# Optimization experiments

Measured on AMD Instinct MI355X. Metric: run time of the kernel, lower is better.

The kernel has to match this reference:

```python
import jax, jax.numpy as jnp
import numpy as np
from jax import lax

M0 = 131072      # total atoms
N_ONEHOT = 92    # one-hot width
N_ENV = 55       # env feature width (so 3*(92-19)+55 = 274 -> final flat dim 324)
N_CRYSTALS = 4096


def _conv1d(x, w, b):
    # x: [N, Cin, L], w: [Cout, Cin, K] -> [N, Cout, L-K+1] (VALID, stride 1)
    y = lax.conv_general_dilated(x, w, window_strides=(1,), padding='VALID',
                                 dimension_numbers=('NCH', 'OIH', 'NCH'))
    return y + b[None, :, None]


def _maxpool2(x):
    # MaxPool1d(kernel=2, stride=2) over last dim
    return lax.reduce_window(x, -jnp.inf, lax.max, (1, 1, 2), (1, 1, 2), 'VALID')


def setup_inputs() -> dict:
    key = jax.random.key(0)
    ks = jax.random.split(key, 12)
    inp = {
        'atom_one_hot': jax.random.uniform(ks[0], (M0, N_ONEHOT), jnp.float32),
        'atom_env': jax.random.normal(ks[1], (M0, N_ENV), jnp.float32),
        'crystal_atom_idx': jnp.sort(jax.random.randint(ks[2], (M0,), 0, N_CRYSTALS)),
        'num_segments': N_CRYSTALS,
        # parameters (PyTorch-style fan-in scaled init)
        'conva_w': jax.random.normal(ks[3], (3, 1, 20), jnp.float32) * 0.2,
        'conva_b': jax.random.normal(ks[4], (3,), jnp.float32) * 0.1,
        'conv1_w': jax.random.normal(ks[5], (3, 1, 20), jnp.float32) * 0.2,
        'conv1_b': jax.random.normal(ks[6], (3,), jnp.float32) * 0.1,
        'conv2_w': jax.random.normal(ks[7], (6, 3, 20), jnp.float32) * 0.1,
        'conv2_b': jax.random.normal(ks[8], (6,), jnp.float32) * 0.1,
        'lin_w': jax.random.normal(ks[9], (32, 324), jnp.float32) * 0.05,
        'lin_b': jnp.zeros((32,), jnp.float32),
        'lin1_w': jax.random.normal(ks[10], (1, 32), jnp.float32) * 0.15,
        'lin1_b': jnp.zeros((1,), jnp.float32),
    }
    return inp


def reference(atom_one_hot, atom_env, crystal_atom_idx, num_segments,
              conva_w, conva_b, conv1_w, conv1_b, conv2_w, conv2_b,
              lin_w, lin_b, lin1_w, lin1_b):
    m0 = atom_one_hot.shape[0]
    # per-atom conv over the one-hot vector
    atom = jax.nn.relu(_conv1d(atom_one_hot[:, None, :], conva_w, conva_b))
    atom = atom.reshape(m0, -1)                       # [m0, 3*(n0-19)]
    total = jnp.concatenate([atom, atom_env], axis=1)[:, None, :]  # [m0, 1, 274]
    one = _maxpool2(jax.nn.relu(_conv1d(total, conv1_w, conv1_b)))   # [m0, 3, 127]
    one = _maxpool2(jax.nn.relu(_conv1d(one, conv2_w, conv2_b)))     # [m0, 6, 54]
    one = one.reshape(m0, -1)                          # [m0, 324]
    # ragged per-crystal mean (segment mean) == sum_atom
    sums = jax.ops.segment_sum(one, crystal_atom_idx, num_segments=num_segments)
    counts = jax.ops.segment_sum(jnp.ones((m0,), one.dtype), crystal_atom_idx,
                                 num_segments=num_segments)
    pooled = sums / jnp.maximum(counts, 1.0)[:, None]  # [n_crystals, 324]
    pooled = jax.nn.relu(pooled)
    h = jax.nn.softplus(pooled @ lin_w.T + lin_b)      # [n_crystals, 32]
    return h @ lin1_w.T + lin1_b                       # [n_crystals, 1]
```

## Files before the change

### kernel.cpp

```cpp
#include <hip/hip_runtime.h>
#include <math.h>

#define M0 131072
#define NC 4096
#define FDIM 324
#define APW 4

#define DSWIN21(w0, w1, w2, w3, w4, g, addr)                                   \
  asm volatile("ds_read2_b64 %0, %6 offset0:0 offset1:1\n\t"                   \
               "ds_read2_b64 %1, %6 offset0:2 offset1:3\n\t"                   \
               "ds_read2_b64 %2, %6 offset0:4 offset1:5\n\t"                   \
               "ds_read2_b64 %3, %6 offset0:6 offset1:7\n\t"                   \
               "ds_read2_b64 %4, %6 offset0:8 offset1:9\n\t"                   \
               "ds_read_b32 %5, %6 offset:80\n\t"                              \
               "s_waitcnt lgkmcnt(0)"                                          \
               : "=v"(w0), "=v"(w1), "=v"(w2), "=v"(w3), "=v"(w4), "=v"(g)     \
               : "v"(addr))

#define DSWIN24(w0, w1, w2, w3, w4, w5, addr)                                  \
  asm volatile("ds_read_b128 %0, %6 offset:0\n\t"                              \
               "ds_read_b128 %1, %6 offset:16\n\t"                             \
               "ds_read_b128 %2, %6 offset:32\n\t"                             \
               "ds_read_b128 %3, %6 offset:48\n\t"                             \
               "ds_read_b128 %4, %6 offset:64\n\t"                             \
               "ds_read_b128 %5, %6 offset:80\n\t"                             \
               "s_waitcnt lgkmcnt(0)"                                          \
               : "=v"(w0), "=v"(w1), "=v"(w2), "=v"(w3), "=v"(w4), "=v"(w5)    \
               : "v"(addr))

#define DSWQ5(q0, q1, q2, q3, q4, addr)                                        \
  asm volatile("ds_read_b128 %0, %5 offset:0\n\t"                              \
               "ds_read_b128 %1, %5 offset:16\n\t"                             \
               "ds_read_b128 %2, %5 offset:32\n\t"                             \
               "ds_read_b128 %3, %5 offset:48\n\t"                             \
               "ds_read_b128 %4, %5 offset:64\n\t"                             \
               "s_waitcnt lgkmcnt(0)"                                          \
               : "=v"(q0), "=v"(q1), "=v"(q2), "=v"(q3), "=v"(q4)              \
               : "v"(addr))

#define DSW64(addr, val)  asm volatile("ds_write_b64 %0, %1" :: "v"(addr), "v"(val))
#define DSW32(addr, val)  asm volatile("ds_write_b32 %0, %1" :: "v"(addr), "v"(val))

template<int J>
__device__ __forceinline__ float el21(const float4 (&W)[5], float g) {
    if constexpr (J >= 20) return g;
    else {
        constexpr int q = J >> 2, r = J & 3;
        if constexpr (r == 0) return W[q].x;
        else if constexpr (r == 1) return W[q].y;
        else if constexpr (r == 2) return W[q].z;
        else return W[q].w;
    }
}
template<int J>
__device__ __forceinline__ float el24(const float4 (&W)[6]) {
    constexpr int q = J >> 2, r = J & 3;
    if constexpr (r == 0) return W[q].x;
    else if constexpr (r == 1) return W[q].y;
    else if constexpr (r == 2) return W[q].z;
    else return W[q].w;
}

template<int K0>
__device__ __forceinline__ void fq2(const float4 wq, const float4 (&W)[5], float g,
                                    float& a0, float& a1) {
    a0 = fmaf(el21<K0 + 0>(W, g), wq.x, a0); a1 = fmaf(el21<K0 + 1>(W, g), wq.x, a1);
    a0 = fmaf(el21<K0 + 1>(W, g), wq.y, a0); a1 = fmaf(el21<K0 + 2>(W, g), wq.y, a1);
    a0 = fmaf(el21<K0 + 2>(W, g), wq.z, a0); a1 = fmaf(el21<K0 + 3>(W, g), wq.z, a1);
    a0 = fmaf(el21<K0 + 3>(W, g), wq.w, a0); a1 = fmaf(el21<K0 + 4>(W, g), wq.w, a1);
}
template<int K0>
__device__ __forceinline__ void fq4(const float4 wq, const float4 (&W)[6], float (&a)[4]) {
    a[0] = fmaf(el24<K0 + 0>(W), wq.x, a[0]); a[1] = fmaf(el24<K0 + 1>(W), wq.x, a[1]);
    a[2] = fmaf(el24<K0 + 2>(W), wq.x, a[2]); a[3] = fmaf(el24<K0 + 3>(W), wq.x, a[3]);
    a[0] = fmaf(el24<K0 + 1>(W), wq.y, a[0]); a[1] = fmaf(el24<K0 + 2>(W), wq.y, a[1]);
    a[2] = fmaf(el24<K0 + 3>(W), wq.y, a[2]); a[3] = fmaf(el24<K0 + 4>(W), wq.y, a[3]);
    a[0] = fmaf(el24<K0 + 2>(W), wq.z, a[0]); a[1] = fmaf(el24<K0 + 3>(W), wq.z, a[1]);
    a[2] = fmaf(el24<K0 + 4>(W), wq.z, a[2]); a[3] = fmaf(el24<K0 + 5>(W), wq.z, a[3]);
    a[0] = fmaf(el24<K0 + 3>(W), wq.w, a[0]); a[1] = fmaf(el24<K0 + 4>(W), wq.w, a[1]);
    a[2] = fmaf(el24<K0 + 5>(W), wq.w, a[2]); a[3] = fmaf(el24<K0 + 6>(W), wq.w, a[3]);
}

__global__ __launch_bounds__(256, 8) void atom_kernel(
    const float* __restrict__ oh_g,
    const float* __restrict__ env_g,
    const int*   __restrict__ idx_g,
    const float* __restrict__ wA, const float* __restrict__ bA,
    const float* __restrict__ w1, const float* __restrict__ b1,
    const float* __restrict__ w2, const float* __restrict__ b2,
    float* __restrict__ sums,
    float* __restrict__ counts)
{
    __shared__ __align__(16) float w_lds[480];
    __shared__ __align__(16) float s_total[4][280];
    __shared__ __align__(16) float s_one1[4][384];

    const int wave = threadIdx.x >> 6;
    const int lane = threadIdx.x & 63;
    const int tid  = threadIdx.x;

    const unsigned w_b   = (unsigned)(size_t)w_lds;
    const unsigned wD_b  = w_b + 480u;
    const unsigned tot_b = (unsigned)(size_t)s_total[wave];
    const unsigned one_b = (unsigned)(size_t)s_one1[wave];
    const unsigned oh_b  = one_b;

    for (int i = tid; i < 360; i += 256) DSW32(w_b + (120u + (unsigned)i) * 4u, w2[i]);
    if (tid < 60)       DSW32(w_b + (unsigned)tid * 4u, wA[tid]);
    else if (tid < 120) DSW32(w_b + (unsigned)tid * 4u, w1[tid - 60]);
    __syncthreads();

    const int wbase = (blockIdx.x * 4 + wave) * APW;

    float fa[6] = {0.f, 0.f, 0.f, 0.f, 0.f, 0.f};
    float cnt = 0.f;
    int cur = idx_g[wbase];

    for (int it = 0; it < APW; ++it) {
        const int atom = wbase + it;
        const int cry = idx_g[atom];
        if (cry != cur) {
            if (lane < 54) {
                float* dst = sums + (size_t)cur * FDIM + lane;
                #pragma unroll
                for (int c2 = 0; c2 < 6; ++c2) {
                    atomicAdd(dst + c2 * 54, fa[c2]);
                    fa[c2] = 0.f;
                }
            }
            if (lane == 0) atomicAdd(&counts[cur], cnt);
            cnt = 0.f;
            cur = cry;
        }

        if (lane < 46) {
            const float2 v = *reinterpret_cast<const float2*>(oh_g + (size_t)atom * 92 + 2 * lane);
            DSW64(oh_b + (unsigned)lane * 8u, v);
        }
        if (lane < 55) {
            const float e = env_g[(size_t)atom * 55 + lane];
            DSW32(tot_b + (219u + (unsigned)lane) * 4u, e);
        }

        if (lane < 37) {
            float4 W[5]; float g;
            DSWIN21(W[0], W[1], W[2], W[3], W[4], g, oh_b + (unsigned)lane * 8u);
            const unsigned p2 = 2u * (unsigned)lane;
            #pragma unroll
            for (int c = 0; c < 3; ++c) {
                float4 wq[5];
                DSWQ5(wq[0], wq[1], wq[2], wq[3], wq[4], w_b + (unsigned)c * 80u);
                float a0 = bA[c], a1 = a0;
                fq2<0>(wq[0], W, g, a0, a1);  fq2<4>(wq[1], W, g, a0, a1);
                fq2<8>(wq[2], W, g, a0, a1);  fq2<12>(wq[3], W, g, a0, a1);
                fq2<16>(wq[4], W, g, a0, a1);
                const unsigned tb = tot_b + (73u * (unsigned)c + p2) * 4u;
                DSW32(tb, fmaxf(a0, 0.f));
                if (p2 + 1 < 73) DSW32(tb + 4u, fmaxf(a1, 0.f));
            }
        }

        {
            float4 W[6];
            DSWIN24(W[0], W[1], W[2], W[3], W[4], W[5], tot_b + (unsigned)lane * 16u);
            #pragma unroll
            for (int c = 0; c < 3; ++c) {
                float4 wq[5];
                DSWQ5(wq[0], wq[1], wq[2], wq[3], wq[4], w_b + 240u + (unsigned)c * 80u);
                float a4[4] = {b1[c], b1[c], b1[c], b1[c]};
                fq4<0>(wq[0], W, a4);  fq4<4>(wq[1], W, a4);  fq4<8>(wq[2], W, a4);
                fq4<12>(wq[3], W, a4); fq4<16>(wq[4], W, a4);
                float2 st;
                st.x = fmaxf(fmaxf(a4[0], a4[1]), 0.f);
                st.y = fmaxf(fmaxf(a4[2], a4[3]), 0.f);
                DSW64(one_b + ((unsigned)c * 128u + 2u * (unsigned)lane) * 4u, st);
            }
        }

        if (lane < 54) {
            float acc0[6], acc1[6];
            #pragma unroll
            for (int c2 = 0; c2 < 6; ++c2) { acc0[c2] = b2[c2]; acc1[c2] = acc0[c2]; }
            #pragma unroll
            for (int ch = 0; ch < 3; ++ch) {
                float4 W[5]; float g;
                DSWIN21(W[0], W[1], W[2], W[3], W[4], g,
                        one_b + (unsigned)ch * 512u + (unsigned)lane * 8u);
                #pragma unroll
                for (int c2 = 0; c2 < 6; ++c2) {
                    float4 wq[5];
                    DSWQ5(wq[0], wq[1], wq[2], wq[3], wq[4],
                          wD_b + ((unsigned)c2 * 3u + (unsigned)ch) * 80u);
                    fq2<0>(wq[0], W, g, acc0[c2], acc1[c2]);
                    fq2<4>(wq[1], W, g, acc0[c2], acc1[c2]);
                    fq2<8>(wq[2], W, g, acc0[c2], acc1[c2]);
                    fq2<12>(wq[3], W, g, acc0[c2], acc1[c2]);
                    fq2<16>(wq[4], W, g, acc0[c2], acc1[c2]);
                }
            }
            #pragma unroll
            for (int c2 = 0; c2 < 6; ++c2)
                fa[c2] += fmaxf(fmaxf(acc0[c2], acc1[c2]), 0.f);
        }
        cnt += 1.f;
    }

    if (lane < 54) {
        float* dst = sums + (size_t)cur * FDIM + lane;
        #pragma unroll
        for (int c2 = 0; c2 < 6; ++c2) atomicAdd(dst + c2 * 54, fa[c2]);
    }
    if (lane == 0) atomicAdd(&counts[cur], cnt);
}

__global__ __launch_bounds__(64) void head_kernel(
    const float* __restrict__ sums, const float* __restrict__ counts,
    const float* __restrict__ lin_w, const float* __restrict__ lin_b,
    const float* __restrict__ lin1_w, const float* __restrict__ lin1_b,
    float* __restrict__ out)
{
    __shared__ float p[FDIM];
    const int c = blockIdx.x;
    const int lane = threadIdx.x;
    const float inv = 1.0f / fmaxf(counts[c], 1.0f);
    for (int i = lane; i < FDIM; i += 64)
        p[i] = fmaxf(sums[(size_t)c * FDIM + i] * inv, 0.f);
    __syncthreads();

    float r = 0.f;
    if (lane < 32) {
        float acc = lin_b[lane];
        const float* wrow = lin_w + lane * FDIM;
        #pragma unroll 4
        for (int i = 0; i < FDIM; ++i) acc = fmaf(p[i], wrow[i], acc);
        const float sp = (acc > 0.f) ? acc + log1pf(expf(-acc)) : log1pf(expf(acc));
        r = sp * lin1_w[lane];
    }
    #pragma unroll
    for (int off = 16; off; off >>= 1) r += __shfl_down(r, off);
    if (lane == 0) out[c] = r + lin1_b[0];
}

extern "C" void kernel_launch(void* const* d_in, const int* in_sizes, int n_in,
                              void* d_out, int out_size, void* d_ws, size_t ws_size,
                              hipStream_t stream) {
    (void)in_sizes; (void)n_in; (void)out_size; (void)ws_size;
    const float* oh    = (const float*)d_in[0];
    const float* env   = (const float*)d_in[1];
    const int*   idx   = (const int*)  d_in[2];
    const float* wA    = (const float*)d_in[4];
    const float* bA    = (const float*)d_in[5];
    const float* w1    = (const float*)d_in[6];
    const float* b1    = (const float*)d_in[7];
    const float* w2    = (const float*)d_in[8];
    const float* b2    = (const float*)d_in[9];
    const float* lin_w = (const float*)d_in[10];
    const float* lin_b = (const float*)d_in[11];
    const float* lin1_w= (const float*)d_in[12];
    const float* lin1_b= (const float*)d_in[13];

    float* sums   = (float*)d_ws;
    float* counts = sums + (size_t)NC * FDIM;

    hipMemsetAsync(d_ws, 0, ((size_t)NC * FDIM + NC) * sizeof(float), stream);

    atom_kernel<<<M0 / (4 * APW), 256, 0, stream>>>(oh, env, idx, wA, bA, w1, b1,
                                                    w2, b2, sums, counts);
    head_kernel<<<NC, 64, 0, stream>>>(sums, counts, lin_w, lin_b, lin1_w, lin1_b,
                                       (float*)d_out);
}
```

Before: 249.3 us.

## Load conv weights via scalar loads into SGPRs instead of LDS broadcast reads

Conv weights are no longer staged in LDS with a block-wide barrier. Each 20-tap filter is now fetched with s_load_dwordx16/x4 into scalar registers and used directly as the uniform FMA operand, which removes the per-lane ds_read_b128 weight traffic and the __syncthreads. The block index is also remapped (blockIdx&7)*1024+(blockIdx>>3), which changes which atoms neighbouring blocks process and may affect cache and atomic locality across XCDs. Each scalar load waits on lgkmcnt(0), so its latency is exposed, and the larger SGPR demand could hurt scheduling.

```diff
diff --git a/kernel.cpp b/kernel.cpp
--- a/kernel.cpp
+++ b/kernel.cpp
@@ -5,6 +5,9 @@
 #define NC 4096
 #define FDIM 324
 #define APW 4
+
+typedef __attribute__((ext_vector_type(16))) float f32x16;
+typedef __attribute__((ext_vector_type(4)))  float f32x4s;
 
 #define DSWIN21(w0, w1, w2, w3, w4, g, addr)                                   \
   asm volatile("ds_read2_b64 %0, %6 offset0:0 offset1:1\n\t"                   \
@@ -28,18 +31,15 @@
                : "=v"(w0), "=v"(w1), "=v"(w2), "=v"(w3), "=v"(w4), "=v"(w5)    \
                : "v"(addr))
 
-#define DSWQ5(q0, q1, q2, q3, q4, addr)                                        \
-  asm volatile("ds_read_b128 %0, %5 offset:0\n\t"                              \
-               "ds_read_b128 %1, %5 offset:16\n\t"                             \
-               "ds_read_b128 %2, %5 offset:32\n\t"                             \
-               "ds_read_b128 %3, %5 offset:48\n\t"                             \
-               "ds_read_b128 %4, %5 offset:64\n\t"                             \
-               "s_waitcnt lgkmcnt(0)"                                          \
-               : "=v"(q0), "=v"(q1), "=v"(q2), "=v"(q3), "=v"(q4)              \
-               : "v"(addr))
-
 #define DSW64(addr, val)  asm volatile("ds_write_b64 %0, %1" :: "v"(addr), "v"(val))
 #define DSW32(addr, val)  asm volatile("ds_write_b32 %0, %1" :: "v"(addr), "v"(val))
+
+#define SLDW20(d16, d4, ptr, O16, O4)                                          \
+  asm volatile("s_load_dwordx16 %0, %2, %3\n\t"                                \
+               "s_load_dwordx4 %1, %2, %4\n\t"                                 \
+               "s_waitcnt lgkmcnt(0)"                                          \
+               : "=&s"(d16), "=&s"(d4)                                         \
+               : "s"(ptr), "n"(O16), "n"(O4))
 
 template<int J>
 __device__ __forceinline__ float el21(const float4 (&W)[5], float g) {
@@ -61,24 +61,48 @@
     else return W[q].w;
 }
 
-template<int K0>
-__device__ __forceinline__ void fq2(const float4 wq, const float4 (&W)[5], float g,
-                                    float& a0, float& a1) {
-    a0 = fmaf(el21<K0 + 0>(W, g), wq.x, a0); a1 = fmaf(el21<K0 + 1>(W, g), wq.x, a1);
-    a0 = fmaf(el21<K0 + 1>(W, g), wq.y, a0); a1 = fmaf(el21<K0 + 2>(W, g), wq.y, a1);
-    a0 = fmaf(el21<K0 + 2>(W, g), wq.z, a0); a1 = fmaf(el21<K0 + 3>(W, g), wq.z, a1);
-    a0 = fmaf(el21<K0 + 3>(W, g), wq.w, a0); a1 = fmaf(el21<K0 + 4>(W, g), wq.w, a1);
-}
-template<int K0>
-__device__ __forceinline__ void fq4(const float4 wq, const float4 (&W)[6], float (&a)[4]) {
-    a[0] = fmaf(el24<K0 + 0>(W), wq.x, a[0]); a[1] = fmaf(el24<K0 + 1>(W), wq.x, a[1]);
-    a[2] = fmaf(el24<K0 + 2>(W), wq.x, a[2]); a[3] = fmaf(el24<K0 + 3>(W), wq.x, a[3]);
-    a[0] = fmaf(el24<K0 + 1>(W), wq.y, a[0]); a[1] = fmaf(el24<K0 + 2>(W), wq.y, a[1]);
-    a[2] = fmaf(el24<K0 + 3>(W), wq.y, a[2]); a[3] = fmaf(el24<K0 + 4>(W), wq.y, a[3]);
-    a[0] = fmaf(el24<K0 + 2>(W), wq.z, a[0]); a[1] = fmaf(el24<K0 + 3>(W), wq.z, a[1]);
-    a[2] = fmaf(el24<K0 + 4>(W), wq.z, a[2]); a[3] = fmaf(el24<K0 + 5>(W), wq.z, a[3]);
-    a[0] = fmaf(el24<K0 + 3>(W), wq.w, a[0]); a[1] = fmaf(el24<K0 + 4>(W), wq.w, a[1]);
-    a[2] = fmaf(el24<K0 + 5>(W), wq.w, a[2]); a[3] = fmaf(el24<K0 + 6>(W), wq.w, a[3]);
+template<int K>
+__device__ __forceinline__ void sfq2(const float wk, const float4 (&W)[5], float g,
+                                     float& a0, float& a1) {
+    a0 = fmaf(el21<K>(W, g),     wk, a0);
+    a1 = fmaf(el21<K + 1>(W, g), wk, a1);
+}
+template<int K>
+__device__ __forceinline__ void sfq4(const float wk, const float4 (&W)[6], float (&a)[4]) {
+    a[0] = fmaf(el24<K>(W),     wk, a[0]);
+    a[1] = fmaf(el24<K + 1>(W), wk, a[1]);
+    a[2] = fmaf(el24<K + 2>(W), wk, a[2]);
+    a[3] = fmaf(el24<K + 3>(W), wk, a[3]);
+}
+
+#define SFQ20_2(S16, S4, W, g, a0, a1) do {                                    \
+  sfq2<0>(S16[0],W,g,a0,a1);  sfq2<1>(S16[1],W,g,a0,a1);                       \
+  sfq2<2>(S16[2],W,g,a0,a1);  sfq2<3>(S16[3],W,g,a0,a1);                       \
+  sfq2<4>(S16[4],W,g,a0,a1);  sfq2<5>(S16[5],W,g,a0,a1);                       \
+  sfq2<6>(S16[6],W,g,a0,a1);  sfq2<7>(S16[7],W,g,a0,a1);                       \
+  sfq2<8>(S16[8],W,g,a0,a1);  sfq2<9>(S16[9],W,g,a0,a1);                       \
+  sfq2<10>(S16[10],W,g,a0,a1); sfq2<11>(S16[11],W,g,a0,a1);                    \
+  sfq2<12>(S16[12],W,g,a0,a1); sfq2<13>(S16[13],W,g,a0,a1);                    \
+  sfq2<14>(S16[14],W,g,a0,a1); sfq2<15>(S16[15],W,g,a0,a1);                    \
+  sfq2<16>(S4[0],W,g,a0,a1);  sfq2<17>(S4[1],W,g,a0,a1);                       \
+  sfq2<18>(S4[2],W,g,a0,a1);  sfq2<19>(S4[3],W,g,a0,a1); } while (0)
+
+#define SFQ20_4(S16, S4, W, a) do {                                            \
+  sfq4<0>(S16[0],W,a);  sfq4<1>(S16[1],W,a);  sfq4<2>(S16[2],W,a);             \
+  sfq4<3>(S16[3],W,a);  sfq4<4>(S16[4],W,a);  sfq4<5>(S16[5],W,a);             \
+  sfq4<6>(S16[6],W,a);  sfq4<7>(S16[7],W,a);  sfq4<8>(S16[8],W,a);             \
+  sfq4<9>(S16[9],W,a);  sfq4<10>(S16[10],W,a); sfq4<11>(S16[11],W,a);          \
+  sfq4<12>(S16[12],W,a); sfq4<13>(S16[13],W,a); sfq4<14>(S16[14],W,a);         \
+  sfq4<15>(S16[15],W,a); sfq4<16>(S4[0],W,a);  sfq4<17>(S4[1],W,a);            \
+  sfq4<18>(S4[2],W,a);  sfq4<19>(S4[3],W,a); } while (0)
+
+template<int IDX>
+__device__ __forceinline__ void d_one(const float* __restrict__ w2p,
+                                      const float4 (&W)[5], float g,
+                                      float& a0, float& a1) {
+    f32x16 s16; f32x4s s4;
+    SLDW20(s16, s4, w2p, IDX * 80, IDX * 80 + 64);
+    SFQ20_2(s16, s4, W, g, a0, a1);
 }
 
 __global__ __launch_bounds__(256, 8) void atom_kernel(
@@ -91,26 +115,20 @@
     float* __restrict__ sums,
     float* __restrict__ counts)
 {
-    __shared__ __align__(16) float w_lds[480];
     __shared__ __align__(16) float s_total[4][280];
     __shared__ __align__(16) float s_one1[4][384];
 
+    const int bid = (blockIdx.x & 7) * 1024 + (blockIdx.x >> 3);
+
     const int wave = threadIdx.x >> 6;
     const int lane = threadIdx.x & 63;
-    const int tid  = threadIdx.x;
-
-    const unsigned w_b   = (unsigned)(size_t)w_lds;
-    const unsigned wD_b  = w_b + 480u;
-    const unsigned tot_b = (unsigned)(size_t)s_total[wave];
-    const unsigned one_b = (unsigned)(size_t)s_one1[wave];
-    const unsigned oh_b  = one_b;
-
-    for (int i = tid; i < 360; i += 256) DSW32(w_b + (120u + (unsigned)i) * 4u, w2[i]);
-    if (tid < 60)       DSW32(w_b + (unsigned)tid * 4u, wA[tid]);
-    else if (tid < 120) DSW32(w_b + (unsigned)tid * 4u, w1[tid - 60]);
-    __syncthreads();
-
-    const int wbase = (blockIdx.x * 4 + wave) * APW;
+
+    const unsigned tot_b = (unsigned)(size_t)&s_total[wave][0];
+    const unsigned one_b = (unsigned)(size_t)&s_one1[wave][0];
+    const unsigned lane8  = (unsigned)lane * 8u;
+    const unsigned lane16 = (unsigned)lane * 16u;
+
+    const int wbase = (bid * 4 + wave) * APW;
 
     float fa[6] = {0.f, 0.f, 0.f, 0.f, 0.f, 0.f};
     float cnt = 0.f;
@@ -135,45 +153,74 @@
 
         if (lane < 46) {
             const float2 v = *reinterpret_cast<const float2*>(oh_g + (size_t)atom * 92 + 2 * lane);
-            DSW64(oh_b + (unsigned)lane * 8u, v);
+            DSW64(one_b + lane8, v);
         }
         if (lane < 55) {
-            const float e = env_g[(size_t)atom * 55 + lane];
-            DSW32(tot_b + (219u + (unsigned)lane) * 4u, e);
+            DSW32(tot_b + (219u + (unsigned)lane) * 4u, env_g[(size_t)atom * 55 + lane]);
         }
 
         if (lane < 37) {
             float4 W[5]; float g;
-            DSWIN21(W[0], W[1], W[2], W[3], W[4], g, oh_b + (unsigned)lane * 8u);
+            DSWIN21(W[0], W[1], W[2], W[3], W[4], g, one_b + lane8);
             const unsigned p2 = 2u * (unsigned)lane;
-            #pragma unroll
-            for (int c = 0; c < 3; ++c) {
-                float4 wq[5];
-                DSWQ5(wq[0], wq[1], wq[2], wq[3], wq[4], w_b + (unsigned)c * 80u);
-                float a0 = bA[c], a1 = a0;
-                fq2<0>(wq[0], W, g, a0, a1);  fq2<4>(wq[1], W, g, a0, a1);
-                fq2<8>(wq[2], W, g, a0, a1);  fq2<12>(wq[3], W, g, a0, a1);
-                fq2<16>(wq[4], W, g, a0, a1);
-                const unsigned tb = tot_b + (73u * (unsigned)c + p2) * 4u;
-                DSW32(tb, fmaxf(a0, 0.f));
-                if (p2 + 1 < 73) DSW32(tb + 4u, fmaxf(a1, 0.f));
+            {
+                f32x16 s16; f32x4s s4;
+                SLDW20(s16, s4, wA, 0, 64);
+                float a0 = bA[0], a1 = a0;
+                SFQ20_2(s16, s4, W, g, a0, a1);
+                DSW32(tot_b + p2 * 4u, fmaxf(a0, 0.f));
+                if (p2 + 1 < 73) DSW32(tot_b + (p2 + 1) * 4u, fmaxf(a1, 0.f));
+            }
+            {
+                f32x16 s16; f32x4s s4;
+                SLDW20(s16, s4, wA, 80, 144);
+                float a0 = bA[1], a1 = a0;
+                SFQ20_2(s16, s4, W, g, a0, a1);
+                DSW32(tot_b + (73u + p2) * 4u, fmaxf(a0, 0.f));
+                if (p2 + 1 < 73) DSW32(tot_b + (74u + p2) * 4u, fmaxf(a1, 0.f));
+            }
+            {
+                f32x16 s16; f32x4s s4;
+                SLDW20(s16, s4, wA, 160, 224);
+                float a0 = bA[2], a1 = a0;
+                SFQ20_2(s16, s4, W, g, a0, a1);
+                DSW32(tot_b + (146u + p2) * 4u, fmaxf(a0, 0.f));
+                if (p2 + 1 < 73) DSW32(tot_b + (147u + p2) * 4u, fmaxf(a1, 0.f));
             }
         }
 
         {
             float4 W[6];
-            DSWIN24(W[0], W[1], W[2], W[3], W[4], W[5], tot_b + (unsigned)lane * 16u);
-            #pragma unroll
-            for (int c = 0; c < 3; ++c) {
-                float4 wq[5];
-                DSWQ5(wq[0], wq[1], wq[2], wq[3], wq[4], w_b + 240u + (unsigned)c * 80u);
-                float a4[4] = {b1[c], b1[c], b1[c], b1[c]};
-                fq4<0>(wq[0], W, a4);  fq4<4>(wq[1], W, a4);  fq4<8>(wq[2], W, a4);
-                fq4<12>(wq[3], W, a4); fq4<16>(wq[4], W, a4);
+            DSWIN24(W[0], W[1], W[2], W[3], W[4], W[5], tot_b + lane16);
+            {
+                f32x16 s16; f32x4s s4;
+                SLDW20(s16, s4, w1, 0, 64);
+                float a4[4] = {b1[0], b1[0], b1[0], b1[0]};
+                SFQ20_4(s16, s4, W, a4);
                 float2 st;
                 st.x = fmaxf(fmaxf(a4[0], a4[1]), 0.f);
                 st.y = fmaxf(fmaxf(a4[2], a4[3]), 0.f);
-                DSW64(one_b + ((unsigned)c * 128u + 2u * (unsigned)lane) * 4u, st);
+                DSW64(one_b + (2u * (unsigned)lane) * 4u, st);
+            }
+            {
+                f32x16 s16; f32x4s s4;
+                SLDW20(s16, s4, w1, 80, 144);
+                float a4[4] = {b1[1], b1[1], b1[1], b1[1]};
+                SFQ20_4(s16, s4, W, a4);
+                float2 st;
+                st.x = fmaxf(fmaxf(a4[0], a4[1]), 0.f);
+                st.y = fmaxf(fmaxf(a4[2], a4[3]), 0.f);
+                DSW64(one_b + (128u + 2u * (unsigned)lane) * 4u, st);
+            }
+            {
+                f32x16 s16; f32x4s s4;
+                SLDW20(s16, s4, w1, 160, 224);
+                float a4[4] = {b1[2], b1[2], b1[2], b1[2]};
+                SFQ20_4(s16, s4, W, a4);
+                float2 st;
+                st.x = fmaxf(fmaxf(a4[0], a4[1]), 0.f);
+                st.y = fmaxf(fmaxf(a4[2], a4[3]), 0.f);
+                DSW64(one_b + (256u + 2u * (unsigned)lane) * 4u, st);
             }
         }
 
@@ -181,22 +228,35 @@
             float acc0[6], acc1[6];
             #pragma unroll
             for (int c2 = 0; c2 < 6; ++c2) { acc0[c2] = b2[c2]; acc1[c2] = acc0[c2]; }
-            #pragma unroll
-            for (int ch = 0; ch < 3; ++ch) {
+            {
                 float4 W[5]; float g;
-                DSWIN21(W[0], W[1], W[2], W[3], W[4], g,
-                        one_b + (unsigned)ch * 512u + (unsigned)lane * 8u);
-                #pragma unroll
-                for (int c2 = 0; c2 < 6; ++c2) {
-                    float4 wq[5];
-                    DSWQ5(wq[0], wq[1], wq[2], wq[3], wq[4],
-                          wD_b + ((unsigned)c2 * 3u + (unsigned)ch) * 80u);
-                    fq2<0>(wq[0], W, g, acc0[c2], acc1[c2]);
-                    fq2<4>(wq[1], W, g, acc0[c2], acc1[c2]);
-                    fq2<8>(wq[2], W, g, acc0[c2], acc1[c2]);
-                    fq2<12>(wq[3], W, g, acc0[c2], acc1[c2]);
-                    fq2<16>(wq[4], W, g, acc0[c2], acc1[c2]);
-                }
+                DSWIN21(W[0], W[1], W[2], W[3], W[4], g, one_b + lane8);
+                d_one<0>(w2, W, g, acc0[0], acc1[0]);
+                d_one<3>(w2, W, g, acc0[1], acc1[1]);
+                d_one<6>(w2, W, g, acc0[2], acc1[2]);
+                d_one<9>(w2, W, g, acc0[3], acc1[3]);
+                d_one<12>(w2, W, g, acc0[4], acc1[4]);
+                d_one<15>(w2, W, g, acc0[5], acc1[5]);
+            }
+            {
+                float4 W[5]; float g;
+                DSWIN21(W[0], W[1], W[2], W[3], W[4], g, one_b + 512u + lane8);
+                d_one<1>(w2, W, g, acc0[0], acc1[0]);
+                d_one<4>(w2, W, g, acc0[1], acc1[1]);
+                d_one<7>(w2, W, g, acc0[2], acc1[2]);
+                d_one<10>(w2, W, g, acc0[3], acc1[3]);
+                d_one<13>(w2, W, g, acc0[4], acc1[4]);
+                d_one<16>(w2, W, g, acc0[5], acc1[5]);
+            }
+            {
+                float4 W[5]; float g;
+                DSWIN21(W[0], W[1], W[2], W[3], W[4], g, one_b + 1024u + lane8);
+                d_one<2>(w2, W, g, acc0[0], acc1[0]);
+                d_one<5>(w2, W, g, acc0[1], acc1[1]);
+                d_one<8>(w2, W, g, acc0[2], acc1[2]);
+                d_one<11>(w2, W, g, acc0[3], acc1[3]);
+                d_one<14>(w2, W, g, acc0[4], acc1[4]);
+                d_one<17>(w2, W, g, acc0[5], acc1[5]);
             }
             #pragma unroll
             for (int c2 = 0; c2 < 6; ++c2)
@@ -264,8 +324,8 @@
 
     hipMemsetAsync(d_ws, 0, ((size_t)NC * FDIM + NC) * sizeof(float), stream);
 
-    atom_kernel<<<M0 / (4 * APW), 256, 0, stream>>>(oh, env, idx, wA, bA, w1, b1,
-                                                    w2, b2, sums, counts);
+    atom_kernel<<<M0 / 16, 256, 0, stream>>>(oh, env, idx, wA, bA, w1, b1,
+                                             w2, b2, sums, counts);
     head_kernel<<<NC, 64, 0, stream>>>(sums, counts, lin_w, lin_b, lin1_w, lin1_b,
                                        (float*)d_out);
 }
```

Measured after the change: 291.2 us. +16.8%, slower.

## Compute conv2 stage with bf16 MFMA instead of scalar FMAs

Applied to the files above, without the earlier changes.

Replaces the scalar FP32 conv2 (3->6 channels, kernel 20) with bf16 16x16x32 MFMA tiles. Conv1 outputs are packed to bf16 in LDS, and conv2 weights are preloaded as A-fragments in registers. Maxpool is done with a lane shuffle and results are staged through an LDS pool buffer before accumulation. Launch bounds occupancy drops from 8 to 4, and bf16 rounding of the activations and weights lowers accuracy.

```diff
diff --git a/kernel.cpp b/kernel.cpp
--- a/kernel.cpp
+++ b/kernel.cpp
@@ -5,6 +5,10 @@
 #define NC 4096
 #define FDIM 324
 #define APW 4
+
+typedef __attribute__((ext_vector_type(8))) short bf16x8;
+typedef __attribute__((ext_vector_type(4))) float f32x4;
+typedef __attribute__((ext_vector_type(4))) int   i32x4;
 
 #define DSWIN21(w0, w1, w2, w3, w4, g, addr)                                   \
   asm volatile("ds_read2_b64 %0, %6 offset0:0 offset1:1\n\t"                   \
@@ -14,7 +18,8 @@
                "ds_read2_b64 %4, %6 offset0:8 offset1:9\n\t"                   \
                "ds_read_b32 %5, %6 offset:80\n\t"                              \
                "s_waitcnt lgkmcnt(0)"                                          \
-               : "=v"(w0), "=v"(w1), "=v"(w2), "=v"(w3), "=v"(w4), "=v"(g)     \
+               : "=&v"(w0), "=&v"(w1), "=&v"(w2), "=&v"(w3), "=&v"(w4),        \
+                 "=&v"(g)                                                      \
                : "v"(addr))
 
 #define DSWIN24(w0, w1, w2, w3, w4, w5, addr)                                  \
@@ -25,21 +30,73 @@
                "ds_read_b128 %4, %6 offset:64\n\t"                             \
                "ds_read_b128 %5, %6 offset:80\n\t"                             \
                "s_waitcnt lgkmcnt(0)"                                          \
-               : "=v"(w0), "=v"(w1), "=v"(w2), "=v"(w3), "=v"(w4), "=v"(w5)    \
-               : "v"(addr))
-
-#define DSWQ5(q0, q1, q2, q3, q4, addr)                                        \
+               : "=&v"(w0), "=&v"(w1), "=&v"(w2), "=&v"(w3), "=&v"(w4),        \
+                 "=&v"(w5)                                                     \
+               : "v"(addr))
+
+#define DSWQ5(q, addr)                                                         \
   asm volatile("ds_read_b128 %0, %5 offset:0\n\t"                              \
                "ds_read_b128 %1, %5 offset:16\n\t"                             \
                "ds_read_b128 %2, %5 offset:32\n\t"                             \
                "ds_read_b128 %3, %5 offset:48\n\t"                             \
                "ds_read_b128 %4, %5 offset:64\n\t"                             \
                "s_waitcnt lgkmcnt(0)"                                          \
-               : "=v"(q0), "=v"(q1), "=v"(q2), "=v"(q3), "=v"(q4)              \
+               : "=&v"(q[0]), "=&v"(q[1]), "=&v"(q[2]), "=&v"(q[3]),           \
+                 "=&v"(q[4])                                                   \
+               : "v"(addr))
+
+#define DSB_G4(q00,q01,q02,q10,q11,q12,q20,q21,q22,q30,q31,q32, addr)          \
+  asm volatile("ds_read2_b32 %0, %12 offset0:0 offset1:1\n\t"                  \
+               "ds_read2_b32 %1, %12 offset0:2 offset1:3\n\t"                  \
+               "ds_read_b32  %2, %12 offset:16\n\t"                            \
+               "ds_read2_b32 %3, %12 offset0:8 offset1:9\n\t"                  \
+               "ds_read2_b32 %4, %12 offset0:10 offset1:11\n\t"                \
+               "ds_read_b32  %5, %12 offset:48\n\t"                            \
+               "ds_read2_b32 %6, %12 offset0:16 offset1:17\n\t"                \
+               "ds_read2_b32 %7, %12 offset0:18 offset1:19\n\t"                \
+               "ds_read_b32  %8, %12 offset:80\n\t"                            \
+               "ds_read2_b32 %9, %12 offset0:24 offset1:25\n\t"                \
+               "ds_read2_b32 %10, %12 offset0:26 offset1:27\n\t"               \
+               "ds_read_b32  %11, %12 offset:112\n\t"                          \
+               "s_waitcnt lgkmcnt(0)"                                          \
+               : "=&v"(q00),"=&v"(q01),"=&v"(q02),"=&v"(q10),"=&v"(q11),       \
+                 "=&v"(q12),"=&v"(q20),"=&v"(q21),"=&v"(q22),"=&v"(q30),       \
+                 "=&v"(q31),"=&v"(q32)                                         \
+               : "v"(addr))
+
+#define DSB_G3(q40,q41,q42,q50,q51,q52,q60,q61,q62, addr)                      \
+  asm volatile("ds_read2_b32 %0, %9 offset0:32 offset1:33\n\t"                 \
+               "ds_read2_b32 %1, %9 offset0:34 offset1:35\n\t"                 \
+               "ds_read_b32  %2, %9 offset:144\n\t"                            \
+               "ds_read2_b32 %3, %9 offset0:40 offset1:41\n\t"                 \
+               "ds_read2_b32 %4, %9 offset0:42 offset1:43\n\t"                 \
+               "ds_read_b32  %5, %9 offset:176\n\t"                            \
+               "ds_read2_b32 %6, %9 offset0:48 offset1:49\n\t"                 \
+               "ds_read2_b32 %7, %9 offset0:50 offset1:51\n\t"                 \
+               "ds_read_b32  %8, %9 offset:208\n\t"                            \
+               "s_waitcnt lgkmcnt(0)"                                          \
+               : "=&v"(q40),"=&v"(q41),"=&v"(q42),"=&v"(q50),"=&v"(q51),       \
+                 "=&v"(q52),"=&v"(q60),"=&v"(q61),"=&v"(q62)                   \
+               : "v"(addr))
+
+#define DSRD6(r0,r1,r2,r3,r4,r5, addr)                                         \
+  asm volatile("ds_read_b32 %0, %6 offset:0\n\t"                               \
+               "ds_read_b32 %1, %6 offset:216\n\t"                             \
+               "ds_read_b32 %2, %6 offset:432\n\t"                             \
+               "ds_read_b32 %3, %6 offset:648\n\t"                             \
+               "ds_read_b32 %4, %6 offset:864\n\t"                             \
+               "ds_read_b32 %5, %6 offset:1080\n\t"                            \
+               "s_waitcnt lgkmcnt(0)"                                          \
+               : "=&v"(r0),"=&v"(r1),"=&v"(r2),"=&v"(r3),"=&v"(r4),"=&v"(r5)   \
                : "v"(addr))
 
 #define DSW64(addr, val)  asm volatile("ds_write_b64 %0, %1" :: "v"(addr), "v"(val))
 #define DSW32(addr, val)  asm volatile("ds_write_b32 %0, %1" :: "v"(addr), "v"(val))
+
+__device__ __forceinline__ unsigned short f2bf(float f) {
+    unsigned u = __builtin_bit_cast(unsigned, f);
+    return (unsigned short)((u + 0x7fffu + ((u >> 16) & 1u)) >> 16);
+}
 
 template<int J>
 __device__ __forceinline__ float el21(const float4 (&W)[5], float g) {
@@ -60,7 +117,6 @@
     else if constexpr (r == 2) return W[q].z;
     else return W[q].w;
 }
-
 template<int K0>
 __device__ __forceinline__ void fq2(const float4 wq, const float4 (&W)[5], float g,
                                     float& a0, float& a1) {
@@ -80,8 +136,58 @@
     a[0] = fmaf(el24<K0 + 3>(W), wq.w, a[0]); a[1] = fmaf(el24<K0 + 4>(W), wq.w, a[1]);
     a[2] = fmaf(el24<K0 + 5>(W), wq.w, a[2]); a[3] = fmaf(el24<K0 + 6>(W), wq.w, a[3]);
 }
-
-__global__ __launch_bounds__(256, 8) void atom_kernel(
+#define FQ2ALL(Q, W, g, a0, a1)                                                \
+  do { fq2<0>(Q[0], W, g, a0, a1);  fq2<4>(Q[1], W, g, a0, a1);                \
+       fq2<8>(Q[2], W, g, a0, a1);  fq2<12>(Q[3], W, g, a0, a1);               \
+       fq2<16>(Q[4], W, g, a0, a1); } while (0)
+
+#define MK_B(bb, p0, p1, p2)                                                   \
+  do {                                                                         \
+    const int _d0 = __builtin_bit_cast(int, (p0).x);                           \
+    const int _d1 = __builtin_bit_cast(int, (p0).y);                           \
+    const int _d2 = __builtin_bit_cast(int, (p1).x);                           \
+    const int _d3 = __builtin_bit_cast(int, (p1).y);                           \
+    const int _d4 = __builtin_bit_cast(int, (p2));                             \
+    i32x4 _b = { (int)__builtin_amdgcn_alignbit((unsigned)_d1, (unsigned)_d0, (unsigned)shf), \
+                 (int)__builtin_amdgcn_alignbit((unsigned)_d2, (unsigned)_d1, (unsigned)shf), \
+                 (int)__builtin_amdgcn_alignbit((unsigned)_d3, (unsigned)_d2, (unsigned)shf), \
+                 (int)__builtin_amdgcn_alignbit((unsigned)_d4, (unsigned)_d3, (unsigned)shf) }; \
+    bb = __builtin_bit_cast(bf16x8, _b);                                       \
+  } while (0)
+
+#define MFMA(A, B, C) __builtin_amdgcn_mfma_f32_16x16x32_bf16((A), (B), (C), 0, 0, 0)
+
+#define D_CH(AF, CH)                                                           \
+  do {                                                                         \
+    const unsigned ab = oneb_b + (unsigned)(CH) * 288u + sdw4;                 \
+    float2 q00,q01,q10,q11,q20,q21,q30,q31; float q02,q12,q22,q32;             \
+    DSB_G4(q00,q01,q02,q10,q11,q12,q20,q21,q22,q30,q31,q32, ab);               \
+    bf16x8 bb;                                                                 \
+    MK_B(bb, q00, q01, q02); t0 = MFMA(AF, bb, t0);                            \
+    MK_B(bb, q10, q11, q12); t1 = MFMA(AF, bb, t1);                            \
+    MK_B(bb, q20, q21, q22); t2 = MFMA(AF, bb, t2);                            \
+    MK_B(bb, q30, q31, q32); t3 = MFMA(AF, bb, t3);                            \
+    float2 q40,q41,q50,q51,q60,q61; float q42,q52,q62;                         \
+    DSB_G3(q40,q41,q42,q50,q51,q52,q60,q61,q62, ab);                           \
+    MK_B(bb, q40, q41, q42); t4 = MFMA(AF, bb, t4);                            \
+    MK_B(bb, q50, q51, q52); t5 = MFMA(AF, bb, t5);                            \
+    MK_B(bb, q60, q61, q62); t6 = MFMA(AF, bb, t6);                            \
+  } while (0)
+
+#define EX_TILE(CT, T)                                                         \
+  do {                                                                         \
+    _Pragma("unroll")                                                          \
+    for (int j = 0; j < 4; ++j) {                                              \
+      const float v = (CT)[j];                                                 \
+      const float w = __shfl_xor(v, 1);                                        \
+      const float m = fmaxf(fmaxf(v, w) + vb[j], 0.f);                         \
+      const int c2i = ((lane >> 4) << 2) + j;                                  \
+      if (!(lane & 1) && c2i < 6 && ((T) < 6 || (lane & 15) < 12))             \
+        DSW32(poolw + (unsigned)(j * 216 + (T) * 32), m);                      \
+    }                                                                          \
+  } while (0)
+
+__global__ __launch_bounds__(256, 4) void atom_kernel(
     const float* __restrict__ oh_g,
     const float* __restrict__ env_g,
     const int*   __restrict__ idx_g,
@@ -91,24 +197,61 @@
     float* __restrict__ sums,
     float* __restrict__ counts)
 {
-    __shared__ __align__(16) float w_lds[480];
+    __shared__ __align__(16) float w_lds[120];
     __shared__ __align__(16) float s_total[4][280];
-    __shared__ __align__(16) float s_one1[4][384];
+    __shared__ __align__(16) float s_oh[4][96];
+    __shared__ __align__(16) unsigned short s_oneb[4][432];
+    __shared__ __align__(16) float s_pool[4][324];
 
     const int wave = threadIdx.x >> 6;
     const int lane = threadIdx.x & 63;
     const int tid  = threadIdx.x;
 
-    const unsigned w_b   = (unsigned)(size_t)w_lds;
-    const unsigned wD_b  = w_b + 480u;
-    const unsigned tot_b = (unsigned)(size_t)s_total[wave];
-    const unsigned one_b = (unsigned)(size_t)s_one1[wave];
-    const unsigned oh_b  = one_b;
-
-    for (int i = tid; i < 360; i += 256) DSW32(w_b + (120u + (unsigned)i) * 4u, w2[i]);
+    const unsigned w_b    = (unsigned)(size_t)w_lds;
+    const unsigned tot_b  = (unsigned)(size_t)&s_total[wave][0];
+    const unsigned oh_b   = (unsigned)(size_t)&s_oh[wave][0];
+    const unsigned oneb_b = (unsigned)(size_t)&s_oneb[wave][0];
+    const unsigned pool_b = (unsigned)(size_t)&s_pool[wave][0];
+    const unsigned lane8  = (unsigned)lane * 8u;
+    const unsigned lane16 = (unsigned)lane * 16u;
+
     if (tid < 60)       DSW32(w_b + (unsigned)tid * 4u, wA[tid]);
-    else if (tid < 120) DSW32(w_b + (unsigned)tid * 4u, w1[tid - 60]);
+    else if (tid < 120) DSW32(w_b + 240u + (unsigned)(tid - 60) * 4u, w1[tid - 60]);
     __syncthreads();
+
+    const int s0  = (lane & 15) + ((lane >> 4) << 3);
+    const int shf = (s0 & 1) << 4;
+    const unsigned sdw4 = (unsigned)(s0 >> 1) << 2;
+    const unsigned qb4  = (unsigned)((lane & 15) >> 1) << 2;
+    const unsigned poolw = pool_b + (unsigned)((lane >> 4) << 2) * 216u + qb4;
+
+    bf16x8 af0{}, af1{}, af2{};
+    {
+        const int r = lane & 15, kb = (lane >> 4) << 3;
+        #pragma unroll
+        for (int j = 0; j < 8; ++j) {
+            const int kk = kb + j;
+            float v0 = 0.f, v1 = 0.f, v2 = 0.f;
+            if (r < 6 && kk < 20) {
+                v0 = w2[r * 60 + kk];
+                v1 = w2[r * 60 + 20 + kk];
+                v2 = w2[r * 60 + 40 + kk];
+            }
+            af0[j] = (short)f2bf(v0);
+            af1[j] = (short)f2bf(v1);
+            af2[j] = (short)f2bf(v2);
+        }
+    }
+    float vb[4];
+    #pragma unroll
+    for (int j = 0; j < 4; ++j) {
+        const int c2i = ((lane >> 4) << 2) + j;
+        float t = 0.f; if (c2i < 6) t = b2[c2i];
+        vb[j] = t;
+    }
+    if (lane < 6)  DSW32(tot_b + (274u + (unsigned)lane) * 4u, 0.f);
+    if (lane < 24) DSW32(oneb_b + (unsigned)(lane >> 3) * 288u + 256u +
+                         (unsigned)(lane & 7) * 4u, 0.f);
 
     const int wbase = (blockIdx.x * 4 + wave) * APW;
 
@@ -135,25 +278,22 @@
 
         if (lane < 46) {
             const float2 v = *reinterpret_cast<const float2*>(oh_g + (size_t)atom * 92 + 2 * lane);
-            DSW64(oh_b + (unsigned)lane * 8u, v);
+            DSW64(oh_b + lane8, v);
         }
         if (lane < 55) {
-            const float e = env_g[(size_t)atom * 55 + lane];
-            DSW32(tot_b + (219u + (unsigned)lane) * 4u, e);
+            DSW32(tot_b + (219u + (unsigned)lane) * 4u, env_g[(size_t)atom * 55 + lane]);
         }
 
         if (lane < 37) {
             float4 W[5]; float g;
-            DSWIN21(W[0], W[1], W[2], W[3], W[4], g, oh_b + (unsigned)lane * 8u);
+            DSWIN21(W[0], W[1], W[2], W[3], W[4], g, oh_b + lane8);
             const unsigned p2 = 2u * (unsigned)lane;
             #pragma unroll
             for (int c = 0; c < 3; ++c) {
                 float4 wq[5];
-                DSWQ5(wq[0], wq[1], wq[2], wq[3], wq[4], w_b + (unsigned)c * 80u);
+                DSWQ5(wq, w_b + (unsigned)c * 80u);
                 float a0 = bA[c], a1 = a0;
-                fq2<0>(wq[0], W, g, a0, a1);  fq2<4>(wq[1], W, g, a0, a1);
-                fq2<8>(wq[2], W, g, a0, a1);  fq2<12>(wq[3], W, g, a0, a1);
-                fq2<16>(wq[4], W, g, a0, a1);
+                FQ2ALL(wq, W, g, a0, a1);
                 const unsigned tb = tot_b + (73u * (unsigned)c + p2) * 4u;
                 DSW32(tb, fmaxf(a0, 0.f));
                 if (p2 + 1 < 73) DSW32(tb + 4u, fmaxf(a1, 0.f));
@@ -162,45 +302,36 @@
 
         {
             float4 W[6];
-            DSWIN24(W[0], W[1], W[2], W[3], W[4], W[5], tot_b + (unsigned)lane * 16u);
+            DSWIN24(W[0], W[1], W[2], W[3], W[4], W[5], tot_b + lane16);
             #pragma unroll
             for (int c = 0; c < 3; ++c) {
                 float4 wq[5];
-                DSWQ5(wq[0], wq[1], wq[2], wq[3], wq[4], w_b + 240u + (unsigned)c * 80u);
+                DSWQ5(wq, w_b + 240u + (unsigned)c * 80u);
                 float a4[4] = {b1[c], b1[c], b1[c], b1[c]};
                 fq4<0>(wq[0], W, a4);  fq4<4>(wq[1], W, a4);  fq4<8>(wq[2], W, a4);
                 fq4<12>(wq[3], W, a4); fq4<16>(wq[4], W, a4);
-                float2 st;
-                st.x = fmaxf(fmaxf(a4[0], a4[1]), 0.f);
-                st.y = fmaxf(fmaxf(a4[2], a4[3]), 0.f);
-                DSW64(one_b + ((unsigned)c * 128u + 2u * (unsigned)lane) * 4u, st);
+                const float p0 = fmaxf(fmaxf(a4[0], a4[1]), 0.f);
+                const float p1 = fmaxf(fmaxf(a4[2], a4[3]), 0.f);
+                const unsigned pk = (unsigned)f2bf(p0) | ((unsigned)f2bf(p1) << 16);
+                DSW32(oneb_b + (unsigned)c * 288u + (unsigned)lane * 4u,
+                      __builtin_bit_cast(float, pk));
             }
         }
 
-        if (lane < 54) {
-            float acc0[6], acc1[6];
-            #pragma unroll
-            for (int c2 = 0; c2 < 6; ++c2) { acc0[c2] = b2[c2]; acc1[c2] = acc0[c2]; }
-            #pragma unroll
-            for (int ch = 0; ch < 3; ++ch) {
-                float4 W[5]; float g;
-                DSWIN21(W[0], W[1], W[2], W[3], W[4], g,
-                        one_b + (unsigned)ch * 512u + (unsigned)lane * 8u);
-                #pragma unroll
-                for (int c2 = 0; c2 < 6; ++c2) {
-                    float4 wq[5];
-                    DSWQ5(wq[0], wq[1], wq[2], wq[3], wq[4],
-                          wD_b + ((unsigned)c2 * 3u + (unsigned)ch) * 80u);
-                    fq2<0>(wq[0], W, g, acc0[c2], acc1[c2]);
-                    fq2<4>(wq[1], W, g, acc0[c2], acc1[c2]);
-                    fq2<8>(wq[2], W, g, acc0[c2], acc1[c2]);
-                    fq2<12>(wq[3], W, g, acc0[c2], acc1[c2]);
-                    fq2<16>(wq[4], W, g, acc0[c2], acc1[c2]);
-                }
+        {
+            f32x4 t0 = {0,0,0,0}, t1 = {0,0,0,0}, t2 = {0,0,0,0}, t3 = {0,0,0,0},
+                  t4 = {0,0,0,0}, t5 = {0,0,0,0}, t6 = {0,0,0,0};
+            D_CH(af0, 0);
+            D_CH(af1, 1);
+            D_CH(af2, 2);
+            EX_TILE(t0, 0); EX_TILE(t1, 1); EX_TILE(t2, 2); EX_TILE(t3, 3);
+            EX_TILE(t4, 4); EX_TILE(t5, 5); EX_TILE(t6, 6);
+            if (lane < 54) {
+                float r0, r1, r2, r3, r4, r5;
+                DSRD6(r0, r1, r2, r3, r4, r5, pool_b + (unsigned)lane * 4u);
+                fa[0] += r0; fa[1] += r1; fa[2] += r2;
+                fa[3] += r3; fa[4] += r4; fa[5] += r5;
             }
-            #pragma unroll
-            for (int c2 = 0; c2 < 6; ++c2)
-                fa[c2] += fmaxf(fmaxf(acc0[c2], acc1[c2]), 0.f);
         }
         cnt += 1.f;
     }
@@ -264,8 +395,8 @@
 
     hipMemsetAsync(d_ws, 0, ((size_t)NC * FDIM + NC) * sizeof(float), stream);
 
-    atom_kernel<<<M0 / (4 * APW), 256, 0, stream>>>(oh, env, idx, wA, bA, w1, b1,
-                                                    w2, b2, sums, counts);
+    atom_kernel<<<M0 / 16, 256, 0, stream>>>(oh, env, idx, wA, bA, w1, b1,
+                                             w2, b2, sums, counts);
     head_kernel<<<NC, 64, 0, stream>>>(sums, counts, lin_w, lin_b, lin1_w, lin1_b,
                                        (float*)d_out);
 }
```

Result: slower. 359.0 us (+44.0%).
